# Performance work log

Measured on AMD Instinct MI355X. Metric: run time of the kernel, lower is better.

## Reference

```python
import jax, jax.numpy as jnp
import numpy as np

K = 3          # kernel size
STRIDE = 1
PAD = 1
GROUPS = 32    # GroupNorm groups
EPS = 1e-5


def setup_inputs() -> dict:
    key = jax.random.key(0)
    ks = jax.random.split(key, 6)
    B, Cin, H, W, Cout = 4, 256, 64, 64, 256
    K2 = K * K
    x = jax.random.normal(ks[0], (B, Cin, H, W), jnp.float32)
    offset = jax.random.normal(ks[1], (B, 2 * K2, H, W), jnp.float32)
    mask = jax.random.uniform(ks[2], (B, K2, H, W), jnp.float32)
    weight = jax.random.normal(ks[3], (Cout, Cin, K, K), jnp.float32) * (1.0 / np.sqrt(Cin * K2))
    bias = jnp.zeros((Cout,), jnp.float32)
    gamma = jnp.ones((Cout,), jnp.float32)   # constant_init(norm, 1)
    beta = jnp.zeros((Cout,), jnp.float32)   # bias=0
    return {"x": x, "offset": offset, "mask": mask, "weight": weight,
            "bias": bias, "gamma": gamma, "beta": beta}


def _modulated_deform_conv(x, offset, mask, weight, bias):
    """DCNv2: bilinear-sample x at learned offsets, modulate by mask, conv-accumulate."""
    B, Cin, H, W = x.shape
    Cout = weight.shape[0]
    K2 = K * K
    Ho = (H + 2 * PAD - K) // STRIDE + 1
    Wo = (W + 2 * PAD - K) // STRIDE + 1

    # base sampling grid per kernel point: [K2, Ho, Wo]
    ky, kx = jnp.meshgrid(jnp.arange(K), jnp.arange(K), indexing='ij')
    ky = ky.reshape(K2).astype(jnp.float32)
    kx = kx.reshape(K2).astype(jnp.float32)
    hs = (jnp.arange(Ho) * STRIDE - PAD).astype(jnp.float32)
    ws = (jnp.arange(Wo) * STRIDE - PAD).astype(jnp.float32)

    off = offset.reshape(B, K2, 2, Ho, Wo)  # interleaved (dy, dx) per kernel point
    y = ky[None, :, None, None] + hs[None, None, :, None] + off[:, :, 0]   # [B,K2,Ho,Wo]
    xc = kx[None, :, None, None] + ws[None, None, None, :] + off[:, :, 1]  # [B,K2,Ho,Wo]

    y0 = jnp.floor(y)
    x0 = jnp.floor(xc)
    dy = y - y0
    dx = xc - x0
    y0i = y0.astype(jnp.int32)
    x0i = x0.astype(jnp.int32)

    x_flat = x.reshape(B, Cin, H * W)

    def corner(yi, xi, w):
        # corner-wise zero padding outside the image (matches mmcv bilinear)
        valid = (yi >= 0) & (yi <= H - 1) & (xi >= 0) & (xi <= W - 1)
        idx = jnp.clip(yi, 0, H - 1) * W + jnp.clip(xi, 0, W - 1)  # [B,K2,Ho,Wo]
        idx_f = idx.reshape(B, -1)
        v = jax.vmap(lambda xf, i: xf[:, i])(x_flat, idx_f)  # [B, Cin, K2*Ho*Wo]
        wv = (w * valid.astype(w.dtype)).reshape(B, 1, -1)
        return v * wv

    val = (corner(y0i,     x0i,     (1 - dy) * (1 - dx))
         + corner(y0i,     x0i + 1, (1 - dy) * dx)
         + corner(y0i + 1, x0i,     dy * (1 - dx))
         + corner(y0i + 1, x0i + 1, dy * dx))
    val = val.reshape(B, Cin, K2, Ho, Wo) * mask[:, None]  # modulate

    w_r = weight.reshape(Cout, Cin, K2)
    out = jnp.einsum('bckhw,ock->bohw', val, w_r) + bias[None, :, None, None]
    return out


def _group_norm(x, gamma, beta):
    B, C, H, W = x.shape
    g = x.reshape(B, GROUPS, C // GROUPS, H, W)
    mu = g.mean(axis=(2, 3, 4), keepdims=True)
    var = ((g - mu) ** 2).mean(axis=(2, 3, 4), keepdims=True)
    g = (g - mu) * jax.lax.rsqrt(var + EPS)
    return g.reshape(B, C, H, W) * gamma[None, :, None, None] + beta[None, :, None, None]


def reference(x, offset, mask, weight, bias, gamma, beta):
    out = _modulated_deform_conv(x, offset, mask, weight, bias)
    out = _group_norm(out, gamma, beta)
    return jax.nn.relu(out)
```

## Files before the change

### kernel.cpp

```cpp
#include <hip/hip_runtime.h>
#include <math.h>

#define BB    4
#define CIN   256
#define HH    64
#define WWID  64
#define COUT  256
#define KKS   3
#define K2    9
#define PADV  1
#define HWSZ  4096
#define GROUPS 32
#define CPG   8
#define EPSV  1e-5f
#define ROWB  4608
#define NKC   36

typedef __attribute__((ext_vector_type(8))) short bf16x8;
typedef __attribute__((ext_vector_type(4))) float f32x4;
typedef __attribute__((ext_vector_type(2))) float f32x2;

#define GLOAD_LDS16(g, l) \
    __builtin_amdgcn_global_load_lds((const __attribute__((address_space(1))) unsigned int*)(g), \
                                     (__attribute__((address_space(3))) unsigned int*)(l), 16, 0, 0)

__device__ __forceinline__ unsigned short f2bf(float f) {
    unsigned u = __float_as_uint(f);
    u = (u + 0x7fffu + ((u >> 16) & 1u)) >> 16;
    return (unsigned short)u;
}
__device__ __forceinline__ f32x2 up2(unsigned q) {
    f32x2 v;
    v.x = __uint_as_float(q << 16);
    v.y = __uint_as_float(q & 0xffff0000u);
    return v;
}
__device__ __forceinline__ unsigned cvtpk(f32x2 f) {
    unsigned r;
    asm("v_cvt_pk_bf16_f32 %0, %1, %2" : "=v"(r) : "v"(f.x), "v"(f.y));
    return r;
}

__global__ __launch_bounds__(256)
void k_pre(const float* __restrict__ x, unsigned short* __restrict__ xh,
           const float* __restrict__ w, unsigned short* __restrict__ wtb,
           float* __restrict__ gstat) {
    int t = threadIdx.x;
    if (blockIdx.x < 128) {
        __shared__ float tile[32][33];
        int hw0 = blockIdx.x * 32;
        int c0  = blockIdx.y * 32;
        int b   = blockIdx.z;
        int tx = t & 31, ty = t >> 5;
        const float* xp = x + (size_t)b * CIN * HWSZ;
        #pragma unroll
        for (int i = 0; i < 4; i++)
            tile[ty + i * 8][tx] = xp[(c0 + ty + i * 8) * HWSZ + hw0 + tx];
        __syncthreads();
        int j = t >> 3, cq = t & 7;
        union { unsigned short s[4]; uint2 d; } pk;
        #pragma unroll
        for (int k = 0; k < 4; k++) pk.s[k] = f2bf(tile[cq * 4 + k][j]);
        *(uint2*)((char*)xh + ((size_t)b * HWSZ * CIN + (size_t)(hw0 + j) * CIN + c0 + cq * 4) * 2) = pk.d;
    } else {
        if (blockIdx.y == 0 && blockIdx.z == 0)
            for (int i = t; i < BB * GROUPS * 2 + 8; i += 256) gstat[i] = 0.f;
        int idx = (blockIdx.y * 4 + blockIdx.z) * 256 + t;
        int co = idx >> 5, c8 = idx & 31;
        int cin0 = c8 * 8;
        int q = c8 >> 3, c = c8 & 7;
        int pc = c ^ (co & 7);
        for (int k2 = 0; k2 < K2; k2++) {
            union { unsigned short s[8]; uint4 qq; } pk;
            #pragma unroll
            for (int j = 0; j < 8; j++)
                pk.s[j] = f2bf(w[(co * CIN + cin0 + j) * K2 + k2]);
            int phys = co * ROWB + k2 * 512 + q * 128 + pc * 16;
            *(uint4*)((char*)wtb + phys) = pk.qq;
        }
    }
}

#define STAGE(dst) do { \
    _Pragma("unroll") \
    for (int i_ = 0; i_ < 4; i_++) \
        GLOAD_LDS16(agb + (size_t)i_ * (64 * (size_t)ROWB), (dst) + i_ * 4096); \
    agb += 128; \
} while (0)

#define GATHER(kn) do { \
    int k2n_ = (kn) >> 2, qn_ = (kn) & 3; \
    int cb_ = (px0 * K2 + k2n_) * 4; \
    int4   ci_ = *(const int4*)&cidx[cb_]; \
    float4 cw_ = *(const float4*)&cwgt[cb_]; \
    gw[0] = cw_.x; gw[1] = cw_.y; gw[2] = cw_.z; gw[3] = cw_.w; \
    const char* xq_ = xb + qn_ * 128; \
    g[0] = *(const uint4*)(xq_ + ci_.x); \
    g[1] = *(const uint4*)(xq_ + ci_.y); \
    g[2] = *(const uint4*)(xq_ + ci_.z); \
    g[3] = *(const uint4*)(xq_ + ci_.w); \
} while (0)

#define PACK(Bdst) do { \
    f32x2 f0 = {0.f, 0.f}, f1 = {0.f, 0.f}, f2 = {0.f, 0.f}, f3 = {0.f, 0.f}; \
    _Pragma("unroll") \
    for (int c_ = 0; c_ < 4; c_++) { \
        f32x2 wv_ = { gw[c_], gw[c_] }; \
        f0 = __builtin_elementwise_fma(wv_, up2(g[c_].x), f0); \
        f1 = __builtin_elementwise_fma(wv_, up2(g[c_].y), f1); \
        f2 = __builtin_elementwise_fma(wv_, up2(g[c_].z), f2); \
        f3 = __builtin_elementwise_fma(wv_, up2(g[c_].w), f3); \
    } \
    uint4 pk_; \
    pk_.x = cvtpk(f0); pk_.y = cvtpk(f1); pk_.z = cvtpk(f2); pk_.w = cvtpk(f3); \
    *(uint4*)&(Bdst)[bofs0] = pk_; \
} while (0)

#define MFMA_STEP(Ac, Bc) do { \
    __builtin_amdgcn_s_setprio(1); \
    _Pragma("unroll") \
    for (int ks_ = 0; ks_ < 2; ks_++) { \
        int up_ = ((ks_ * 4 + hf) ^ skey) * 8; \
        bf16x8 af_[4], bv_[2]; \
        _Pragma("unroll") \
        for (int mi_ = 0; mi_ < 4; mi_++) \
            af_[mi_] = *(const bf16x8*)&(Ac)[(wm * 64 + mi_ * 16 + r16) * 64 + up_]; \
        _Pragma("unroll") \
        for (int ni_ = 0; ni_ < 2; ni_++) \
            bv_[ni_] = *(const bf16x8*)&(Bc)[(wn * 32 + ni_ * 16 + r16) * 64 + up_]; \
        _Pragma("unroll") \
        for (int mi_ = 0; mi_ < 4; mi_++) \
            _Pragma("unroll") \
            for (int ni_ = 0; ni_ < 2; ni_++) \
                acc[mi_][ni_] = __builtin_amdgcn_mfma_f32_16x16x32_bf16( \
                    af_[mi_], bv_[ni_], acc[mi_][ni_], 0, 0, 0); \
    } \
    __builtin_amdgcn_s_setprio(0); \
} while (0)

#define BODY(kc, Ac, An, Bc, Bn, lAn) do { \
    if ((kc) + 1 < NKC) { \
        STAGE(lAn); \
        GATHER((kc) + 1); \
        __builtin_amdgcn_sched_barrier(0); \
    } \
    MFMA_STEP(Ac, Bc); \
    if ((kc) + 1 < NKC) { \
        PACK(Bn); \
        __syncthreads(); \
    } \
} while (0)

__global__ __launch_bounds__(512, 2)
void k_conv(const unsigned short* __restrict__ wtb, const unsigned short* __restrict__ xh,
            const float* __restrict__ offset, const float* __restrict__ mask,
            const float* __restrict__ bias, float* __restrict__ out,
            float* __restrict__ gstat) {
    __shared__ __align__(16) unsigned short As[2][256 * 64];
    __shared__ __align__(16) unsigned short Bs[2][64 * 64];
    __shared__ __align__(16) int   cidx[64 * K2 * 4];
    __shared__ __align__(16) float cwgt[64 * K2 * 4];
    __shared__ float gs[32], gss[32];

    int lid = blockIdx.x;
    int strip = (lid & 7) * 32 + (lid >> 3);
    int b = strip >> 6;
    int hwbase = (strip & 63) * 64;

    int t = threadIdx.x, w = t >> 6, l = t & 63;
    int r16 = l & 15, hf = l >> 4;
    int skey = r16 & 7;
    int wm = w & 3, wn = w >> 2;

    if (t < 32) { gs[t] = 0.f; gss[t] = 0.f; }

    for (int i = t; i < 64 * K2; i += 512) {
        int px = i / K2, k2 = i - px * K2;
        int hw = hwbase + px;
        int ho = hw >> 6, wo = hw & 63;
        int ky = k2 / KKS, kx = k2 - ky * KKS;
        float dy = offset[((b * (2 * K2) + k2 * 2 + 0) * HWSZ) + hw];
        float dx = offset[((b * (2 * K2) + k2 * 2 + 1) * HWSZ) + hw];
        float m  = mask[(b * K2 + k2) * HWSZ + hw];
        float y  = (float)(ky + ho - PADV) + dy;
        float xc = (float)(kx + wo - PADV) + dx;
        float y0f = floorf(y), x0f = floorf(xc);
        float fy = y - y0f, fx = xc - x0f;
        int y0 = (int)y0f, x0 = (int)x0f;
        int   yy[2] = { y0, y0 + 1 };
        int   xx[2] = { x0, x0 + 1 };
        float wy[2] = { 1.f - fy, fy };
        float wx[2] = { 1.f - fx, fx };
        #pragma unroll
        for (int ii = 0; ii < 2; ii++)
            #pragma unroll
            for (int jj = 0; jj < 2; jj++) {
                int yi = yy[ii], xi = xx[jj];
                bool valid = (yi >= 0) && (yi < HH) && (xi >= 0) && (xi < WWID);
                int yc  = min(max(yi, 0), HH - 1);
                int xcc = min(max(xi, 0), WWID - 1);
                cidx[i * 4 + ii * 2 + jj] = (yc * WWID + xcc) << 9;
                cwgt[i * 4 + ii * 2 + jj] = valid ? (wy[ii] * wx[jj] * m) : 0.f;
            }
    }

    const char* agb = (const char*)wtb + (size_t)(t >> 3) * ROWB + (t & 7) * 16;
    unsigned short* lA0 = &As[0][t * 8];
    unsigned short* lA1 = &As[1][t * 8];

    int sc  = t & 7;
    int px0 = t >> 3;
    const char* xb = (const char*)xh + (size_t)b * HWSZ * CIN * 2 + sc * 16;
    int bofs0 = px0 * 64 + (sc ^ (px0 & 7)) * 8;

    f32x4 acc[4][2];
    #pragma unroll
    for (int mi = 0; mi < 4; mi++)
        #pragma unroll
        for (int ni = 0; ni < 2; ni++) acc[mi][ni] = (f32x4)0.f;

    __syncthreads();

    uint4 g[4]; float gw[4];
    GATHER(0);
    STAGE(lA0);
    PACK(Bs[0]);
    __syncthreads();

    for (int kc2 = 0; kc2 < NKC; kc2 += 2) {
        BODY(kc2,     As[0], As[1], Bs[0], Bs[1], lA1);
        BODY(kc2 + 1, As[1], As[0], Bs[1], Bs[0], lA0);
    }

    float s4[4] = {0,0,0,0}, ss4[4] = {0,0,0,0};
    #pragma unroll
    for (int mi = 0; mi < 4; mi++) {
        #pragma unroll
        for (int r = 0; r < 4; r++) {
            int co = wm * 64 + mi * 16 + hf * 4 + r;
            float bs = bias[co];
            float* orow = out + ((size_t)(b * COUT + co)) * HWSZ;
            #pragma unroll
            for (int ni = 0; ni < 2; ni++) {
                int n = hwbase + wn * 32 + ni * 16 + r16;
                float v = acc[mi][ni][r] + bs;
                orow[n] = v;
                s4[mi] += v; ss4[mi] += v * v;
            }
        }
    }
    int gb = hf >> 1;
    #pragma unroll
    for (int mi = 0; mi < 4; mi++) {
        atomicAdd(&gs [wm * 8 + mi * 2 + gb], s4[mi]);
        atomicAdd(&gss[wm * 8 + mi * 2 + gb], ss4[mi]);
    }
    __syncthreads();
    if (t < 32) {
        atomicAdd(&gstat[(b * GROUPS + t) * 2 + 0], gs[t]);
        atomicAdd(&gstat[(b * GROUPS + t) * 2 + 1], gss[t]);
    }
}

__global__ __launch_bounds__(256)
void k_gnfinal(float* __restrict__ out, const float* __restrict__ gstat,
               const float* __restrict__ gamma, const float* __restrict__ beta) {
    int i4 = blockIdx.x * 256 + threadIdx.x;
    int e  = i4 * 4;
    int c  = (e >> 12) & 255;
    int b  = e >> 20;
    int g  = c >> 3;
    float s  = gstat[((b * GROUPS) + g) * 2 + 0];
    float ss = gstat[((b * GROUPS) + g) * 2 + 1];
    const float inv = 1.f / (float)(CPG * HWSZ);
    float mu  = s * inv;
    float var = ss * inv - mu * mu;
    float rstd = rsqrtf(var + EPSV);
    float ga = gamma[c] * rstd;
    float be = beta[c] - mu * ga;
    float4 v = ((float4*)out)[i4];
    v.x = fmaxf(v.x * ga + be, 0.f);
    v.y = fmaxf(v.y * ga + be, 0.f);
    v.z = fmaxf(v.z * ga + be, 0.f);
    v.w = fmaxf(v.w * ga + be, 0.f);
    ((float4*)out)[i4] = v;
}

extern "C" void kernel_launch(void* const* d_in, const int* in_sizes, int n_in,
                              void* d_out, int out_size, void* d_ws, size_t ws_size,
                              hipStream_t stream) {
    const float* x      = (const float*)d_in[0];
    const float* offset = (const float*)d_in[1];
    const float* mask   = (const float*)d_in[2];
    const float* weight = (const float*)d_in[3];
    const float* bias   = (const float*)d_in[4];
    const float* gamma  = (const float*)d_in[5];
    const float* beta   = (const float*)d_in[6];
    float* out = (float*)d_out;

    unsigned short* xh    = (unsigned short*)d_ws;
    unsigned short* wtb   = xh + (size_t)4194304;
    float*          gstat = (float*)(wtb + (size_t)589824);

    k_pre<<<dim3(129, 8, 4), 256, 0, stream>>>(x, xh, weight, wtb, gstat);
    k_conv<<<256, 512, 0, stream>>>(wtb, xh, offset, mask, bias, out, gstat);
    k_gnfinal<<<(size_t)BB * COUT * HWSZ / 1024, 256, 0, stream>>>(out, gstat, gamma, beta);
}
```

Measured before the change: 152.0 us.

## Load weight fragments directly into registers in MFMA layout, drop LDS A staging

```diff
diff --git a/kernel.cpp b/kernel.cpp
--- a/kernel.cpp
+++ b/kernel.cpp
@@ -13,16 +13,11 @@
 #define GROUPS 32
 #define CPG   8
 #define EPSV  1e-5f
-#define ROWB  4608
 #define NKC   36
 
 typedef __attribute__((ext_vector_type(8))) short bf16x8;
 typedef __attribute__((ext_vector_type(4))) float f32x4;
 typedef __attribute__((ext_vector_type(2))) float f32x2;
-
-#define GLOAD_LDS16(g, l) \
-    __builtin_amdgcn_global_load_lds((const __attribute__((address_space(1))) unsigned int*)(g), \
-                                     (__attribute__((address_space(3))) unsigned int*)(l), 16, 0, 0)
 
 __device__ __forceinline__ unsigned short f2bf(float f) {
     unsigned u = __float_as_uint(f);
@@ -46,85 +41,85 @@
            const float* __restrict__ w, unsigned short* __restrict__ wtb,
            float* __restrict__ gstat) {
     int t = threadIdx.x;
-    if (blockIdx.x < 128) {
-        __shared__ float tile[32][33];
-        int hw0 = blockIdx.x * 32;
+    if (blockIdx.x < 64) {
+        __shared__ float tile[32][65];
+        int hw0 = blockIdx.x * 64;
         int c0  = blockIdx.y * 32;
         int b   = blockIdx.z;
-        int tx = t & 31, ty = t >> 5;
         const float* xp = x + (size_t)b * CIN * HWSZ;
-        #pragma unroll
-        for (int i = 0; i < 4; i++)
-            tile[ty + i * 8][tx] = xp[(c0 + ty + i * 8) * HWSZ + hw0 + tx];
+        int col = t & 63, r0 = t >> 6;
+        #pragma unroll
+        for (int i = 0; i < 8; i++)
+            tile[i * 4 + r0][col] = xp[(c0 + i * 4 + r0) * HWSZ + hw0 + col];
         __syncthreads();
-        int j = t >> 3, cq = t & 7;
-        union { unsigned short s[4]; uint2 d; } pk;
-        #pragma unroll
-        for (int k = 0; k < 4; k++) pk.s[k] = f2bf(tile[cq * 4 + k][j]);
-        *(uint2*)((char*)xh + ((size_t)b * HWSZ * CIN + (size_t)(hw0 + j) * CIN + c0 + cq * 4) * 2) = pk.d;
+        int hw = t >> 2, cq = t & 3;
+        union { unsigned short s[8]; uint4 qq; } pk;
+        #pragma unroll
+        for (int k = 0; k < 8; k++) pk.s[k] = f2bf(tile[cq * 8 + k][hw]);
+        *(uint4*)((char*)xh + (((size_t)b * HWSZ + hw0 + hw) * CIN + c0 + cq * 8) * 2) = pk.qq;
     } else {
         if (blockIdx.y == 0 && blockIdx.z == 0)
             for (int i = t; i < BB * GROUPS * 2 + 8; i += 256) gstat[i] = 0.f;
         int idx = (blockIdx.y * 4 + blockIdx.z) * 256 + t;
         int co = idx >> 5, c8 = idx & 31;
-        int cin0 = c8 * 8;
-        int q = c8 >> 3, c = c8 & 7;
-        int pc = c ^ (co & 7);
+        int q  = c8 >> 3;
+        int ks = (c8 & 7) >> 2;
+        int hf = c8 & 3;
+        int lane16 = hf * 16 + (co & 15);
         for (int k2 = 0; k2 < K2; k2++) {
+            int kc = k2 * 4 + q;
             union { unsigned short s[8]; uint4 qq; } pk;
             #pragma unroll
             for (int j = 0; j < 8; j++)
-                pk.s[j] = f2bf(w[(co * CIN + cin0 + j) * K2 + k2]);
-            int phys = co * ROWB + k2 * 512 + q * 128 + pc * 16;
+                pk.s[j] = f2bf(w[(co * CIN + c8 * 8 + j) * K2 + k2]);
+            size_t phys = (size_t)(((co >> 4) * 36 + kc)) * 2048 + ks * 1024 + lane16 * 16;
             *(uint4*)((char*)wtb + phys) = pk.qq;
         }
     }
 }
 
-#define STAGE(dst) do { \
-    _Pragma("unroll") \
-    for (int i_ = 0; i_ < 4; i_++) \
-        GLOAD_LDS16(agb + (size_t)i_ * (64 * (size_t)ROWB), (dst) + i_ * 4096); \
-    agb += 128; \
-} while (0)
-
-#define GATHER(kn) do { \
+#define GATHER2(garr, gwarr, kn) do { \
     int k2n_ = (kn) >> 2, qn_ = (kn) & 3; \
     int cb_ = (px0 * K2 + k2n_) * 4; \
     int4   ci_ = *(const int4*)&cidx[cb_]; \
     float4 cw_ = *(const float4*)&cwgt[cb_]; \
-    gw[0] = cw_.x; gw[1] = cw_.y; gw[2] = cw_.z; gw[3] = cw_.w; \
+    gwarr[0] = cw_.x; gwarr[1] = cw_.y; gwarr[2] = cw_.z; gwarr[3] = cw_.w; \
     const char* xq_ = xb + qn_ * 128; \
-    g[0] = *(const uint4*)(xq_ + ci_.x); \
-    g[1] = *(const uint4*)(xq_ + ci_.y); \
-    g[2] = *(const uint4*)(xq_ + ci_.z); \
-    g[3] = *(const uint4*)(xq_ + ci_.w); \
-} while (0)
-
-#define PACK(Bdst) do { \
+    garr[0] = *(const uint4*)(xq_ + ci_.x); \
+    garr[1] = *(const uint4*)(xq_ + ci_.y); \
+    garr[2] = *(const uint4*)(xq_ + ci_.z); \
+    garr[3] = *(const uint4*)(xq_ + ci_.w); \
+} while (0)
+
+#define ISSUE_A(Ar) do { \
+    Ar[0] = *(const bf16x8*)(ap0);        Ar[1] = *(const bf16x8*)(ap0 + 1024); \
+    Ar[2] = *(const bf16x8*)(ap1);        Ar[3] = *(const bf16x8*)(ap1 + 1024); \
+    Ar[4] = *(const bf16x8*)(ap2);        Ar[5] = *(const bf16x8*)(ap2 + 1024); \
+    Ar[6] = *(const bf16x8*)(ap3);        Ar[7] = *(const bf16x8*)(ap3 + 1024); \
+    ap0 += 2048; ap1 += 2048; ap2 += 2048; ap3 += 2048; \
+} while (0)
+
+#define PACK(garr, gwarr, Bdst) do { \
     f32x2 f0 = {0.f, 0.f}, f1 = {0.f, 0.f}, f2 = {0.f, 0.f}, f3 = {0.f, 0.f}; \
     _Pragma("unroll") \
     for (int c_ = 0; c_ < 4; c_++) { \
-        f32x2 wv_ = { gw[c_], gw[c_] }; \
-        f0 = __builtin_elementwise_fma(wv_, up2(g[c_].x), f0); \
-        f1 = __builtin_elementwise_fma(wv_, up2(g[c_].y), f1); \
-        f2 = __builtin_elementwise_fma(wv_, up2(g[c_].z), f2); \
-        f3 = __builtin_elementwise_fma(wv_, up2(g[c_].w), f3); \
+        f32x2 wv_ = { gwarr[c_], gwarr[c_] }; \
+        f0 = __builtin_elementwise_fma(wv_, up2(garr[c_].x), f0); \
+        f1 = __builtin_elementwise_fma(wv_, up2(garr[c_].y), f1); \
+        f2 = __builtin_elementwise_fma(wv_, up2(garr[c_].z), f2); \
+        f3 = __builtin_elementwise_fma(wv_, up2(garr[c_].w), f3); \
     } \
     uint4 pk_; \
     pk_.x = cvtpk(f0); pk_.y = cvtpk(f1); pk_.z = cvtpk(f2); pk_.w = cvtpk(f3); \
     *(uint4*)&(Bdst)[bofs0] = pk_; \
 } while (0)
 
-#define MFMA_STEP(Ac, Bc) do { \
+#define MFMA_STEP(Ar, Bc) do { \
     __builtin_amdgcn_s_setprio(1); \
     _Pragma("unroll") \
     for (int ks_ = 0; ks_ < 2; ks_++) { \
         int up_ = ((ks_ * 4 + hf) ^ skey) * 8; \
-        bf16x8 af_[4], bv_[2]; \
-        _Pragma("unroll") \
-        for (int mi_ = 0; mi_ < 4; mi_++) \
-            af_[mi_] = *(const bf16x8*)&(Ac)[(wm * 64 + mi_ * 16 + r16) * 64 + up_]; \
+        bf16x8 bv_[2]; \
         _Pragma("unroll") \
         for (int ni_ = 0; ni_ < 2; ni_++) \
             bv_[ni_] = *(const bf16x8*)&(Bc)[(wn * 32 + ni_ * 16 + r16) * 64 + up_]; \
@@ -133,22 +128,24 @@
             _Pragma("unroll") \
             for (int ni_ = 0; ni_ < 2; ni_++) \
                 acc[mi_][ni_] = __builtin_amdgcn_mfma_f32_16x16x32_bf16( \
-                    af_[mi_], bv_[ni_], acc[mi_][ni_], 0, 0, 0); \
+                    Ar[mi_ * 2 + ks_], bv_[ni_], acc[mi_][ni_], 0, 0, 0); \
     } \
     __builtin_amdgcn_s_setprio(0); \
 } while (0)
 
-#define BODY(kc, Ac, An, Bc, Bn, lAn) do { \
-    if ((kc) + 1 < NKC) { \
-        STAGE(lAn); \
-        GATHER((kc) + 1); \
-        __builtin_amdgcn_sched_barrier(0); \
-    } \
-    MFMA_STEP(Ac, Bc); \
-    if ((kc) + 1 < NKC) { \
-        PACK(Bn); \
-        __syncthreads(); \
-    } \
+#define LGKM_BAR() do { \
+    asm volatile("s_waitcnt lgkmcnt(0)\n\ts_barrier" ::: "memory"); \
+    __builtin_amdgcn_sched_barrier(0); \
+} while (0)
+
+#define BODY(kc, Acur, Anxt, Bcur, Bnxt, gU, gwU, gF, gwF) do { \
+    ISSUE_A(Anxt); \
+    GATHER2(gF, gwF, (kc) + 2); \
+    __builtin_amdgcn_sched_barrier(0); \
+    MFMA_STEP(Acur, Bcur); \
+    __builtin_amdgcn_sched_barrier(0); \
+    PACK(gU, gwU, Bnxt); \
+    LGKM_BAR(); \
 } while (0)
 
 __global__ __launch_bounds__(512, 2)
@@ -156,7 +153,6 @@
             const float* __restrict__ offset, const float* __restrict__ mask,
             const float* __restrict__ bias, float* __restrict__ out,
             float* __restrict__ gstat) {
-    __shared__ __align__(16) unsigned short As[2][256 * 64];
     __shared__ __align__(16) unsigned short Bs[2][64 * 64];
     __shared__ __align__(16) int   cidx[64 * K2 * 4];
     __shared__ __align__(16) float cwgt[64 * K2 * 4];
@@ -204,9 +200,11 @@
             }
     }
 
-    const char* agb = (const char*)wtb + (size_t)(t >> 3) * ROWB + (t & 7) * 16;
-    unsigned short* lA0 = &As[0][t * 8];
-    unsigned short* lA1 = &As[1][t * 8];
+    const char* wb = (const char*)wtb + (size_t)l * 16;
+    const char* ap0 = wb + (size_t)((wm * 4 + 0) * 36) * 2048;
+    const char* ap1 = wb + (size_t)((wm * 4 + 1) * 36) * 2048;
+    const char* ap2 = wb + (size_t)((wm * 4 + 2) * 36) * 2048;
+    const char* ap3 = wb + (size_t)((wm * 4 + 3) * 36) * 2048;
 
     int sc  = t & 7;
     int px0 = t >> 3;
@@ -221,16 +219,28 @@
 
     __syncthreads();
 
-    uint4 g[4]; float gw[4];
-    GATHER(0);
-    STAGE(lA0);
-    PACK(Bs[0]);
-    __syncthreads();
-
-    for (int kc2 = 0; kc2 < NKC; kc2 += 2) {
-        BODY(kc2,     As[0], As[1], Bs[0], Bs[1], lA1);
-        BODY(kc2 + 1, As[1], As[0], Bs[1], Bs[0], lA0);
-    }
+    uint4 gA[4], gB[4]; float gwA[4], gwB[4];
+    bf16x8 Aa[8], Ab[8];
+    GATHER2(gA, gwA, 0);
+    ISSUE_A(Aa);
+    GATHER2(gB, gwB, 1);
+    PACK(gA, gwA, Bs[0]);
+    LGKM_BAR();
+
+    unsigned short* Bs0 = &Bs[0][0];
+    unsigned short* Bs1 = &Bs[1][0];
+
+    for (int kc2 = 0; kc2 < 34; kc2 += 2) {
+        BODY(kc2,     Aa, Ab, Bs0, Bs1, gB, gwB, gA, gwA);
+        BODY(kc2 + 1, Ab, Aa, Bs1, Bs0, gA, gwA, gB, gwB);
+    }
+    ISSUE_A(Ab);
+    __builtin_amdgcn_sched_barrier(0);
+    MFMA_STEP(Aa, Bs0);
+    __builtin_amdgcn_sched_barrier(0);
+    PACK(gB, gwB, Bs1);
+    LGKM_BAR();
+    MFMA_STEP(Ab, Bs1);
 
     float s4[4] = {0,0,0,0}, ss4[4] = {0,0,0,0};
     #pragma unroll
@@ -302,7 +312,7 @@
     unsigned short* wtb   = xh + (size_t)4194304;
     float*          gstat = (float*)(wtb + (size_t)589824);
 
-    k_pre<<<dim3(129, 8, 4), 256, 0, stream>>>(x, xh, weight, wtb, gstat);
+    k_pre<<<dim3(65, 8, 4), 256, 0, stream>>>(x, xh, weight, wtb, gstat);
     k_conv<<<256, 512, 0, stream>>>(wtb, xh, offset, mask, bias, out, gstat);
     k_gnfinal<<<(size_t)BB * COUT * HWSZ / 1024, 256, 0, stream>>>(out, gstat, gamma, beta);
 }
```

After: 146.2 us. 1.04x faster.
